# Kernel optimization log

Measured on AMD Instinct MI355X. Metric: run time of the kernel, lower is better.

## Reference

```python
import jax, jax.numpy as jnp
import numpy as np

N_NODES = 1000000
N_EDGES = 2000000
VOCAB = 202        # 200 known codes + 2 specials
MAX_ISN_SIZE = 15
N_REL = 3
DIMS = [36, 24, 16, 8, 4]  # 4 + 32 concat input, then RGCN stack


def setup_inputs() -> dict:
    key = jax.random.key(0)
    ks = jax.random.split(key, 20)
    s = 0.1
    inp = {}
    inp["x_code"] = jax.random.randint(ks[0], (N_NODES,), 0, VOCAB)
    inp["x_size"] = jax.random.randint(ks[1], (N_NODES,), 0, MAX_ISN_SIZE)
    inp["edge_index"] = jax.random.randint(ks[2], (2, N_EDGES), 0, N_NODES)
    inp["edge_type"] = jax.random.randint(ks[3], (N_EDGES,), 0, N_REL)
    inp["size_emb"] = jax.random.normal(ks[4], (MAX_ISN_SIZE, 4), dtype=jnp.float32) * s
    inp["code_emb"] = jax.random.normal(ks[5], (VOCAB, 32), dtype=jnp.float32) * s
    for i in range(4):
        inp[f"w{i}"] = jax.random.normal(ks[6 + 3 * i], (N_REL, DIMS[i], DIMS[i + 1]), dtype=jnp.float32) * s
        inp[f"root{i}"] = jax.random.normal(ks[7 + 3 * i], (DIMS[i], DIMS[i + 1]), dtype=jnp.float32) * s
        inp[f"b{i}"] = jnp.zeros((DIMS[i + 1],), dtype=jnp.float32)
    inp["lin_w"] = jax.random.normal(ks[18], (4, 2), dtype=jnp.float32) * s
    inp["lin_b"] = jnp.zeros((2,), dtype=jnp.float32)
    return inp


def _rgcn(x, src, dst, edge_type, weight, root, bias, n):
    # PyG RGCNConv: out[i] = bias + x[i] @ root + sum_r mean_{j in N_r(i)} x[j] @ W_r
    out = x @ root + bias
    for r in range(N_REL):
        mask = (edge_type == r).astype(x.dtype)            # [E]
        msg = (x @ weight[r])[src] * mask[:, None]          # [E, out]
        ssum = jax.ops.segment_sum(msg, dst, num_segments=n)
        cnt = jax.ops.segment_sum(mask, dst, num_segments=n)
        out = out + ssum / jnp.maximum(cnt, 1.0)[:, None]
    return out


def reference(x_code, x_size, edge_index, edge_type, size_emb, code_emb,
              w0, root0, b0, w1, root1, b1, w2, root2, b2, w3, root3, b3,
              lin_w, lin_b):
    n = x_code.shape[0]
    src, dst = edge_index[0], edge_index[1]
    x = jnp.concatenate([size_emb[x_size], code_emb[x_code]], axis=1)  # [N, 36]
    for w, root, b in ((w0, root0, b0), (w1, root1, b1), (w2, root2, b2), (w3, root3, b3)):
        x = jax.nn.relu(_rgcn(x, src, dst, edge_type, w, root, b, n))
    return x @ lin_w + lin_b  # [N, 2]
```

## Files before the change

### kernel.cpp

```cpp
#include <hip/hip_runtime.h>
#include <hip/hip_fp16.h>

#define NREL 3
#define EPB 2048
#define BKT_SHIFT 10
#define BKT_MASK ((1 << BKT_SHIFT) - 1)

__device__ __forceinline__ void unpack8(uint4 v, float* o) {
    *(float2*)(o+0) = __half22float2(*(__half2*)&v.x);
    *(float2*)(o+2) = __half22float2(*(__half2*)&v.y);
    *(float2*)(o+4) = __half22float2(*(__half2*)&v.z);
    *(float2*)(o+6) = __half22float2(*(__half2*)&v.w);
}
__device__ __forceinline__ unsigned pack2(float a, float b) {
    __half2 h = __floats2half2_rn(a, b);
    return *(unsigned*)&h;
}

__global__ void k_tables2(const float* __restrict__ size_emb,
                          const float* __restrict__ code_emb,
                          const float* __restrict__ w0,
                          const float* __restrict__ root0,
                          const float* __restrict__ b0,
                          float* __restrict__ T, float* __restrict__ Troot,
                          int ns, int nc)
{
    int ntype = ns * nc;
    int tid = blockIdx.x * blockDim.x + threadIdx.x;
    int tot1 = NREL * ntype * 24;
    if (tid < tot1) {
        int d = tid % 24;
        int sc = (tid / 24) % ntype;
        int r = tid / (24 * ntype);
        int sz = sc / nc, cd = sc % nc;
        float a = 0.f;
        #pragma unroll
        for (int k = 0; k < 4; ++k)  a += size_emb[sz*4+k] * w0[(r*36+k)*24+d];
        for (int k = 0; k < 32; ++k) a += code_emb[cd*32+k] * w0[(r*36+4+k)*24+d];
        T[tid] = a;
    } else if (tid < tot1 + ntype * 24) {
        int t = tid - tot1;
        int d = t % 24;
        int sc = t / 24;
        int sz = sc / nc, cd = sc % nc;
        float a = b0[d];
        #pragma unroll
        for (int k = 0; k < 4; ++k)  a += size_emb[sz*4+k] * root0[k*24+d];
        for (int k = 0; k < 32; ++k) a += code_emb[cd*32+k] * root0[(4+k)*24+d];
        Troot[t] = a;
    }
}

__global__ void k_key(const int* __restrict__ x_size, const int* __restrict__ x_code,
                      int* __restrict__ key2, int n, int nc)
{
    int i = blockIdx.x * blockDim.x + threadIdx.x;
    if (i < n) key2[i] = x_size[i] * nc + x_code[i];
}

__global__ void __launch_bounds__(256) k_hist(
    const int* __restrict__ dst, int* __restrict__ histT, int E, int NB, int NBK)
{
    __shared__ int h[1 << BKT_SHIFT];
    int bl = blockIdx.x;
    for (int t = threadIdx.x; t < (1 << BKT_SHIFT); t += 256) h[t] = 0;
    __syncthreads();
    int base = bl * EPB;
    #pragma unroll
    for (int it = 0; it < EPB / 256; ++it) {
        int e = base + it * 256 + (int)threadIdx.x;
        if (e < E) atomicAdd(&h[dst[e] >> BKT_SHIFT], 1);
    }
    __syncthreads();
    for (int b = threadIdx.x; b < NB; b += 256)
        histT[b * NBK + bl] = h[b];
}

__global__ void kscan1(const int* __restrict__ arr, int* __restrict__ partials, int m)
{
    __shared__ int s[256];
    int t = threadIdx.x;
    int base = blockIdx.x * 1024 + t * 4;
    int sum = 0;
    #pragma unroll
    for (int j = 0; j < 4; ++j) {
        int i = base + j;
        if (i < m) sum += arr[i];
    }
    s[t] = sum; __syncthreads();
    for (int off = 128; off > 0; off >>= 1) {
        if (t < off) s[t] += s[t + off];
        __syncthreads();
    }
    if (t == 0) partials[blockIdx.x] = s[0];
}

__global__ void kscan2(int* partials, int np)
{
    __shared__ int s[1024];
    int t = threadIdx.x;
    int v = (t < np) ? partials[t] : 0;
    s[t] = v; __syncthreads();
    for (int off = 1; off < 1024; off <<= 1) {
        int a = (t >= off) ? s[t - off] : 0;
        __syncthreads();
        s[t] += a; __syncthreads();
    }
    if (t < np) partials[t] = s[t] - v;
}

__global__ void kscan3(int* __restrict__ arr, const int* __restrict__ partials, int m)
{
    __shared__ int s[256];
    int t = threadIdx.x;
    int base = blockIdx.x * 1024 + t * 4;
    int d0 = 0, d1 = 0, d2 = 0, d3 = 0;
    if (base + 0 < m) d0 = arr[base+0];
    if (base + 1 < m) d1 = arr[base+1];
    if (base + 2 < m) d2 = arr[base+2];
    if (base + 3 < m) d3 = arr[base+3];
    int tsum = d0 + d1 + d2 + d3;
    s[t] = tsum; __syncthreads();
    for (int off = 1; off < 256; off <<= 1) {
        int a = (t >= off) ? s[t - off] : 0;
        __syncthreads();
        s[t] += a; __syncthreads();
    }
    int excl = s[t] - tsum + partials[blockIdx.x];
    if (base + 0 < m) arr[base+0] = excl;
    if (base + 1 < m) arr[base+1] = excl + d0;
    if (base + 2 < m) arr[base+2] = excl + d0 + d1;
    if (base + 3 < m) arr[base+3] = excl + d0 + d1 + d2;
}

__global__ void __launch_bounds__(256) k_scatter(
    const int* __restrict__ src, const int* __restrict__ dst,
    const int* __restrict__ et, const int* __restrict__ offT,
    unsigned* __restrict__ tmp, int E, int NB, int NBK)
{
    __shared__ int h[1 << BKT_SHIFT];
    int bl = blockIdx.x;
    for (int t = threadIdx.x; t < (1 << BKT_SHIFT); t += 256) h[t] = 0;
    __syncthreads();
    int base = bl * EPB;
    #pragma unroll
    for (int it = 0; it < EPB / 256; ++it) {
        int e = base + it * 256 + (int)threadIdx.x;
        if (e < E) {
            int d = dst[e];
            int b = d >> BKT_SHIFT;
            int rank = atomicAdd(&h[b], 1);
            int pos = offT[b * NBK + bl] + rank;
            tmp[pos] = (unsigned)src[e] | ((unsigned)et[e] << 20)
                     | ((unsigned)(d & BKT_MASK) << 22);
        }
    }
}

__global__ void __launch_bounds__(256) k_csr(
    const unsigned* __restrict__ tmp, const int* __restrict__ offT,
    int* __restrict__ rowptr, unsigned* __restrict__ edges,
    int n, int E, int NB, int NBK)
{
    __shared__ int cnt[1 << BKT_SHIFT];
    __shared__ int fil[1 << BKT_SHIFT];
    __shared__ int ws[256];
    int b = blockIdx.x;
    int eb = offT[b * NBK];
    int ee = (b + 1 < NB) ? offT[(b + 1) * NBK] : E;
    int node0 = b << BKT_SHIFT;

    for (int t = threadIdx.x; t < (1 << BKT_SHIFT); t += 256) cnt[t] = 0;
    __syncthreads();
    for (int e = eb + (int)threadIdx.x; e < ee; e += 256)
        atomicAdd(&cnt[tmp[e] >> 22], 1);
    __syncthreads();

    int t = threadIdx.x;
    int c0 = cnt[4*t+0], c1 = cnt[4*t+1], c2 = cnt[4*t+2], c3 = cnt[4*t+3];
    int tsum = c0 + c1 + c2 + c3;
    ws[t] = tsum; __syncthreads();
    for (int off = 1; off < 256; off <<= 1) {
        int a = (t >= off) ? ws[t - off] : 0;
        __syncthreads();
        ws[t] += a; __syncthreads();
    }
    int excl = ws[t] - tsum;
    fil[4*t+0] = excl;
    fil[4*t+1] = excl + c0;
    fil[4*t+2] = excl + c0 + c1;
    fil[4*t+3] = excl + c0 + c1 + c2;
    __syncthreads();

    for (int l = threadIdx.x; l < (1 << BKT_SHIFT); l += 256) {
        int node = node0 + l;
        if (node < n) rowptr[node] = eb + fil[l];
    }
    if (b == NB - 1 && threadIdx.x == 0) rowptr[n] = E;
    __syncthreads();

    for (int e = eb + (int)threadIdx.x; e < ee; e += 256) {
        unsigned w = tmp[e];
        int l = w >> 22;
        int pos = eb + atomicAdd(&fil[l], 1);
        edges[pos] = w & 0x3FFFFF;
    }
}

__global__ void __launch_bounds__(256) k_layer0_pull(
    const int* __restrict__ key2,
    const int* __restrict__ rowptr, const unsigned* __restrict__ edges,
    const float* __restrict__ T,
    const float* __restrict__ Troot,
    __half* __restrict__ xout, int n, int ntype)
{
    int i = blockIdx.x * blockDim.x + threadIdx.x;
    if (i >= n) return;

    int e0 = rowptr[i], e1 = rowptr[i+1];
    int c0 = 0, c1 = 0, c2 = 0;
    for (int e = e0; e < e1; ++e) {
        int r = edges[e] >> 20;
        c0 += (r == 0); c1 += (r == 1); c2 += (r == 2);
    }
    float inv0 = 1.f / fmaxf((float)c0, 1.f);
    float inv1 = 1.f / fmaxf((float)c1, 1.f);
    float inv2 = 1.f / fmaxf((float)c2, 1.f);

    float acc[24];
    {
        const float4* tr = (const float4*)(Troot + (size_t)key2[i] * 24);
        #pragma unroll
        for (int q = 0; q < 6; ++q) {
            float4 v = tr[q];
            acc[q*4+0]=v.x; acc[q*4+1]=v.y; acc[q*4+2]=v.z; acc[q*4+3]=v.w;
        }
    }
    for (int e = e0; e < e1; ++e) {
        unsigned sl = edges[e];
        int s = sl & 0xFFFFF;
        int r = sl >> 20;
        float w = (r == 0) ? inv0 : ((r == 1) ? inv1 : inv2);
        const float4* trow = (const float4*)(T + ((size_t)r * ntype + key2[s]) * 24);
        #pragma unroll
        for (int q = 0; q < 6; ++q) {
            float4 v = trow[q];
            acc[q*4+0] = fmaf(v.x, w, acc[q*4+0]);
            acc[q*4+1] = fmaf(v.y, w, acc[q*4+1]);
            acc[q*4+2] = fmaf(v.z, w, acc[q*4+2]);
            acc[q*4+3] = fmaf(v.w, w, acc[q*4+3]);
        }
    }
    unsigned ow[12];
    #pragma unroll
    for (int q = 0; q < 12; ++q)
        ow[q] = pack2(fmaxf(acc[2*q], 0.f), fmaxf(acc[2*q+1], 0.f));
    uint4* op = (uint4*)(xout + (size_t)i * 24);
    #pragma unroll
    for (int q = 0; q < 3; ++q) op[q] = ((uint4*)ow)[q];
}

template<int DIN, int DOUT, bool FINAL>
__global__ void __launch_bounds__(256) k_layer_pull(
    const __half* __restrict__ xin,
    __half* __restrict__ xout,
    const int* __restrict__ rowptr, const unsigned* __restrict__ edges,
    const float* __restrict__ W,
    const float* __restrict__ root,
    const float* __restrict__ bias,
    const float* __restrict__ linw,
    const float* __restrict__ linb,
    float* __restrict__ finout, int n)
{
    int j = blockIdx.x * blockDim.x + threadIdx.x;
    if (j >= n) return;

    float a0[DIN], a1[DIN], a2[DIN];
    #pragma unroll
    for (int k = 0; k < DIN; ++k) { a0[k] = 0.f; a1[k] = 0.f; a2[k] = 0.f; }
    int c0 = 0, c1 = 0, c2 = 0;

    int e0 = rowptr[j], e1 = rowptr[j+1];
    for (int e = e0; e < e1; ++e) {
        unsigned sl = edges[e];
        int s = sl & 0xFFFFF;
        int r = sl >> 20;
        const uint4* p = (const uint4*)(xin + (size_t)s * DIN);
        float xs[DIN];
        #pragma unroll
        for (int q = 0; q < DIN/8; ++q) unpack8(p[q], xs + q*8);
        if (r == 0) {
            ++c0;
            #pragma unroll
            for (int k = 0; k < DIN; ++k) a0[k] += xs[k];
        } else if (r == 1) {
            ++c1;
            #pragma unroll
            for (int k = 0; k < DIN; ++k) a1[k] += xs[k];
        } else {
            ++c2;
            #pragma unroll
            for (int k = 0; k < DIN; ++k) a2[k] += xs[k];
        }
    }
    {
        float inv0 = 1.f / fmaxf((float)c0, 1.f);
        float inv1 = 1.f / fmaxf((float)c1, 1.f);
        float inv2 = 1.f / fmaxf((float)c2, 1.f);
        #pragma unroll
        for (int k = 0; k < DIN; ++k) { a0[k] *= inv0; a1[k] *= inv1; a2[k] *= inv2; }
    }

    float o[DOUT];
    #pragma unroll
    for (int d = 0; d < DOUT; ++d) o[d] = bias[d];

    {
        const uint4* p = (const uint4*)(xin + (size_t)j * DIN);
        float xi[DIN];
        #pragma unroll
        for (int q = 0; q < DIN/8; ++q) unpack8(p[q], xi + q*8);
        #pragma unroll
        for (int k = 0; k < DIN; ++k) {
            #pragma unroll
            for (int d = 0; d < DOUT; ++d)
                o[d] = fmaf(xi[k], root[k*DOUT + d], o[d]);
        }
    }
    #pragma unroll
    for (int k = 0; k < DIN; ++k) {
        #pragma unroll
        for (int d = 0; d < DOUT; ++d)
            o[d] = fmaf(a0[k], W[(0*DIN + k)*DOUT + d], o[d]);
    }
    #pragma unroll
    for (int k = 0; k < DIN; ++k) {
        #pragma unroll
        for (int d = 0; d < DOUT; ++d)
            o[d] = fmaf(a1[k], W[(1*DIN + k)*DOUT + d], o[d]);
    }
    #pragma unroll
    for (int k = 0; k < DIN; ++k) {
        #pragma unroll
        for (int d = 0; d < DOUT; ++d)
            o[d] = fmaf(a2[k], W[(2*DIN + k)*DOUT + d], o[d]);
    }
    #pragma unroll
    for (int d = 0; d < DOUT; ++d) o[d] = fmaxf(o[d], 0.f);

    if (FINAL) {
        float o0 = linb[0], o1 = linb[1];
        #pragma unroll
        for (int k = 0; k < 4; ++k) {
            o0 = fmaf(o[k], linw[k*2+0], o0);
            o1 = fmaf(o[k], linw[k*2+1], o1);
        }
        *(float2*)(finout + (size_t)j * 2) = make_float2(o0, o1);
    } else {
        unsigned ow[DOUT/2];
        #pragma unroll
        for (int q = 0; q < DOUT/2; ++q) ow[q] = pack2(o[2*q], o[2*q+1]);
        uint4* op = (uint4*)(xout + (size_t)j * DOUT);
        #pragma unroll
        for (int q = 0; q < DOUT/8; ++q) op[q] = ((uint4*)ow)[q];
    }
}

extern "C" void kernel_launch(void* const* d_in, const int* in_sizes, int n_in,
                              void* d_out, int out_size, void* d_ws, size_t ws_size,
                              hipStream_t stream)
{
    const int*   x_code    = (const int*)d_in[0];
    const int*   x_size    = (const int*)d_in[1];
    const int*   edge_index= (const int*)d_in[2];
    const int*   edge_type = (const int*)d_in[3];
    const float* size_emb  = (const float*)d_in[4];
    const float* code_emb  = (const float*)d_in[5];
    const float* w0 = (const float*)d_in[6];  const float* root0 = (const float*)d_in[7];  const float* b0 = (const float*)d_in[8];
    const float* w1 = (const float*)d_in[9];  const float* root1 = (const float*)d_in[10]; const float* b1 = (const float*)d_in[11];
    const float* w2 = (const float*)d_in[12]; const float* root2 = (const float*)d_in[13]; const float* b2 = (const float*)d_in[14];
    const float* w3 = (const float*)d_in[15]; const float* root3 = (const float*)d_in[16]; const float* b3 = (const float*)d_in[17];
    const float* lin_w = (const float*)d_in[18];
    const float* lin_b = (const float*)d_in[19];

    int n  = in_sizes[0];
    int E  = in_sizes[3];
    int ns = in_sizes[4] / 4;
    int nc = in_sizes[5] / 32;
    int ntype = ns * nc;
    const int* esrc = edge_index;
    const int* edst = edge_index + E;

    int NB  = (n + BKT_MASK) >> BKT_SHIFT;
    int NBK = (E + EPB - 1) / EPB;
    int m   = NB * NBK;

    char* ws = (char*)d_ws;
    size_t off = 0;
    auto alloc = [&](size_t bytes) -> void* {
        void* p = ws + off;
        off = (off + bytes + 255) & ~(size_t)255;
        return p;
    };
    __half*   bufA     = (__half*)  alloc((size_t)n * 24 * 2);
    __half*   bufB     = (__half*)  alloc((size_t)n * 16 * 2);
    int*      rowptr   = (int*)     alloc(((size_t)n + 1) * 4);
    unsigned* edges    = (unsigned*)alloc((size_t)E * 4);
    unsigned* tmp      = (unsigned*)alloc((size_t)E * 4);
    int*      histT    = (int*)     alloc((size_t)m * 4);
    int*      key2     = (int*)     alloc((size_t)n * 4);
    int*      partials = (int*)     alloc(4096 * 4);
    float*    T        = (float*)   alloc((size_t)NREL * ntype * 24 * 4);
    float*    Troot    = (float*)   alloc((size_t)ntype * 24 * 4);

    const int tb = 256;
    int tableThreads = NREL*ntype*24 + ntype*24;
    k_tables2<<<(tableThreads + tb - 1)/tb, tb, 0, stream>>>(
        size_emb, code_emb, w0, root0, b0, T, Troot, ns, nc);
    k_key<<<(n + tb - 1)/tb, tb, 0, stream>>>(x_size, x_code, key2, n, nc);

    k_hist<<<NBK, tb, 0, stream>>>(edst, histT, E, NB, NBK);
    int nblk = (m + 1023) / 1024;
    kscan1<<<nblk, tb, 0, stream>>>(histT, partials, m);
    kscan2<<<1, 1024, 0, stream>>>(partials, nblk);
    kscan3<<<nblk, tb, 0, stream>>>(histT, partials, m);
    k_scatter<<<NBK, tb, 0, stream>>>(esrc, edst, edge_type, histT, tmp, E, NB, NBK);
    k_csr<<<NB, tb, 0, stream>>>(tmp, histT, rowptr, edges, n, E, NB, NBK);

    int g256 = (n + 255) / 256;
    k_layer0_pull<<<g256, tb, 0, stream>>>(key2, rowptr, edges, T, Troot, bufA, n, ntype);
    k_layer_pull<24,16,false><<<g256, tb, 0, stream>>>(bufA, bufB, rowptr, edges,
                                                 w1, root1, b1, nullptr, nullptr, nullptr, n);
    k_layer_pull<16, 8,false><<<g256, tb, 0, stream>>>(bufB, bufA, rowptr, edges,
                                                 w2, root2, b2, nullptr, nullptr, nullptr, n);
    k_layer_pull< 8, 4,true ><<<g256, tb, 0, stream>>>(bufA, nullptr, rowptr, edges,
                                                 w3, root3, b3, lin_w, lin_b, (float*)d_out, n);
}
```

Before: 432.6 us.

## Precompute source type keys into compact edge array and widen buckets

The scatter pass now looks up each edge's source type key once and packs it, together with the relation, into a 16-bit per-edge array that layer 0 reads. This removes layer 0's dependent random gather of key2[src]. Buckets widen from 1024 to 4096 nodes, so the histogram uses 256 bins and the CSR build scans 16 counts per thread. Layer-1 input rows are padded to 32 halves (64 B) for aligned gathers, which adds memory traffic, and the scatter pass does extra random reads and writes 8-byte temp entries.

```diff
diff --git a/kernel.cpp b/kernel.cpp
--- a/kernel.cpp
+++ b/kernel.cpp
@@ -3,8 +3,10 @@
 
 #define NREL 3
 #define EPB 2048
-#define BKT_SHIFT 10
-#define BKT_MASK ((1 << BKT_SHIFT) - 1)
+#define BKT_SHIFT 12
+#define BKT_NODES (1 << BKT_SHIFT)
+#define BKT_MASK (BKT_NODES - 1)
+#define X1S 32
 
 __device__ __forceinline__ void unpack8(uint4 v, float* o) {
     *(float2*)(o+0) = __half22float2(*(__half2*)&v.x);
@@ -61,9 +63,9 @@
 __global__ void __launch_bounds__(256) k_hist(
     const int* __restrict__ dst, int* __restrict__ histT, int E, int NB, int NBK)
 {
-    __shared__ int h[1 << BKT_SHIFT];
+    __shared__ int h[256];
     int bl = blockIdx.x;
-    for (int t = threadIdx.x; t < (1 << BKT_SHIFT); t += 256) h[t] = 0;
+    h[threadIdx.x] = 0;
     __syncthreads();
     int base = bl * EPB;
     #pragma unroll
@@ -72,8 +74,8 @@
         if (e < E) atomicAdd(&h[dst[e] >> BKT_SHIFT], 1);
     }
     __syncthreads();
-    for (int b = threadIdx.x; b < NB; b += 256)
-        histT[b * NBK + bl] = h[b];
+    if ((int)threadIdx.x < NB)
+        histT[threadIdx.x * NBK + bl] = h[threadIdx.x];
 }
 
 __global__ void kscan1(const int* __restrict__ arr, int* __restrict__ partials, int m)
@@ -135,12 +137,13 @@
 
 __global__ void __launch_bounds__(256) k_scatter(
     const int* __restrict__ src, const int* __restrict__ dst,
-    const int* __restrict__ et, const int* __restrict__ offT,
-    unsigned* __restrict__ tmp, int E, int NB, int NBK)
-{
-    __shared__ int h[1 << BKT_SHIFT];
+    const int* __restrict__ et, const int* __restrict__ key2,
+    const int* __restrict__ offT,
+    uint2* __restrict__ tmp, int E, int NB, int NBK)
+{
+    __shared__ int h[256];
     int bl = blockIdx.x;
-    for (int t = threadIdx.x; t < (1 << BKT_SHIFT); t += 256) h[t] = 0;
+    h[threadIdx.x] = 0;
     __syncthreads();
     int base = bl * EPB;
     #pragma unroll
@@ -149,67 +152,80 @@
         if (e < E) {
             int d = dst[e];
             int b = d >> BKT_SHIFT;
+            int s = src[e];
+            int r = et[e];
+            int tk = key2[s];
             int rank = atomicAdd(&h[b], 1);
             int pos = offT[b * NBK + bl] + rank;
-            tmp[pos] = (unsigned)src[e] | ((unsigned)et[e] << 20)
-                     | ((unsigned)(d & BKT_MASK) << 22);
+            tmp[pos] = make_uint2((unsigned)s | ((unsigned)r << 20),
+                                  (unsigned)(d & BKT_MASK)
+                                | ((unsigned)tk << 12)
+                                | ((unsigned)r << 24));
         }
     }
 }
 
 __global__ void __launch_bounds__(256) k_csr(
-    const unsigned* __restrict__ tmp, const int* __restrict__ offT,
+    const uint2* __restrict__ tmp, const int* __restrict__ offT,
     int* __restrict__ rowptr, unsigned* __restrict__ edges,
+    unsigned short* __restrict__ edges0,
     int n, int E, int NB, int NBK)
 {
-    __shared__ int cnt[1 << BKT_SHIFT];
-    __shared__ int fil[1 << BKT_SHIFT];
+    __shared__ int cnt[BKT_NODES];
+    __shared__ int fil[BKT_NODES];
     __shared__ int ws[256];
     int b = blockIdx.x;
     int eb = offT[b * NBK];
     int ee = (b + 1 < NB) ? offT[(b + 1) * NBK] : E;
     int node0 = b << BKT_SHIFT;
-
-    for (int t = threadIdx.x; t < (1 << BKT_SHIFT); t += 256) cnt[t] = 0;
-    __syncthreads();
-    for (int e = eb + (int)threadIdx.x; e < ee; e += 256)
-        atomicAdd(&cnt[tmp[e] >> 22], 1);
-    __syncthreads();
-
     int t = threadIdx.x;
-    int c0 = cnt[4*t+0], c1 = cnt[4*t+1], c2 = cnt[4*t+2], c3 = cnt[4*t+3];
-    int tsum = c0 + c1 + c2 + c3;
-    ws[t] = tsum; __syncthreads();
-    for (int off = 1; off < 256; off <<= 1) {
-        int a = (t >= off) ? ws[t - off] : 0;
-        __syncthreads();
-        ws[t] += a; __syncthreads();
-    }
-    int excl = ws[t] - tsum;
-    fil[4*t+0] = excl;
-    fil[4*t+1] = excl + c0;
-    fil[4*t+2] = excl + c0 + c1;
-    fil[4*t+3] = excl + c0 + c1 + c2;
-    __syncthreads();
-
-    for (int l = threadIdx.x; l < (1 << BKT_SHIFT); l += 256) {
+
+    for (int l = t; l < BKT_NODES; l += 256) cnt[l] = 0;
+    __syncthreads();
+    for (int e = eb + t; e < ee; e += 256)
+        atomicAdd(&cnt[tmp[e].y & BKT_MASK], 1);
+    __syncthreads();
+
+    {
+        int base16 = t * 16;
+        int sum = 0;
+        #pragma unroll
+        for (int j = 0; j < 16; ++j) sum += cnt[base16 + j];
+        ws[t] = sum; __syncthreads();
+        for (int off = 1; off < 256; off <<= 1) {
+            int a = (t >= off) ? ws[t - off] : 0;
+            __syncthreads();
+            ws[t] += a; __syncthreads();
+        }
+        int run = ws[t] - sum;
+        #pragma unroll
+        for (int j = 0; j < 16; ++j) {
+            int c = cnt[base16 + j];
+            fil[base16 + j] = run;
+            run += c;
+        }
+    }
+    __syncthreads();
+
+    for (int l = t; l < BKT_NODES; l += 256) {
         int node = node0 + l;
         if (node < n) rowptr[node] = eb + fil[l];
     }
-    if (b == NB - 1 && threadIdx.x == 0) rowptr[n] = E;
-    __syncthreads();
-
-    for (int e = eb + (int)threadIdx.x; e < ee; e += 256) {
-        unsigned w = tmp[e];
-        int l = w >> 22;
+    if (b == NB - 1 && t == 0) rowptr[n] = E;
+    __syncthreads();
+
+    for (int e = eb + t; e < ee; e += 256) {
+        uint2 w = tmp[e];
+        int l = w.y & BKT_MASK;
         int pos = eb + atomicAdd(&fil[l], 1);
-        edges[pos] = w & 0x3FFFFF;
+        edges[pos]  = w.x;
+        edges0[pos] = (unsigned short)(w.y >> 12);
     }
 }
 
 __global__ void __launch_bounds__(256) k_layer0_pull(
     const int* __restrict__ key2,
-    const int* __restrict__ rowptr, const unsigned* __restrict__ edges,
+    const int* __restrict__ rowptr, const unsigned short* __restrict__ edges0,
     const float* __restrict__ T,
     const float* __restrict__ Troot,
     __half* __restrict__ xout, int n, int ntype)
@@ -220,7 +236,7 @@
     int e0 = rowptr[i], e1 = rowptr[i+1];
     int c0 = 0, c1 = 0, c2 = 0;
     for (int e = e0; e < e1; ++e) {
-        int r = edges[e] >> 20;
+        int r = edges0[e] >> 12;
         c0 += (r == 0); c1 += (r == 1); c2 += (r == 2);
     }
     float inv0 = 1.f / fmaxf((float)c0, 1.f);
@@ -237,11 +253,11 @@
         }
     }
     for (int e = e0; e < e1; ++e) {
-        unsigned sl = edges[e];
-        int s = sl & 0xFFFFF;
-        int r = sl >> 20;
+        unsigned short sl = edges0[e];
+        int tk = sl & 0xFFF;
+        int r  = sl >> 12;
         float w = (r == 0) ? inv0 : ((r == 1) ? inv1 : inv2);
-        const float4* trow = (const float4*)(T + ((size_t)r * ntype + key2[s]) * 24);
+        const float4* trow = (const float4*)(T + ((size_t)r * ntype + tk) * 24);
         #pragma unroll
         for (int q = 0; q < 6; ++q) {
             float4 v = trow[q];
@@ -251,16 +267,17 @@
             acc[q*4+3] = fmaf(v.w, w, acc[q*4+3]);
         }
     }
-    unsigned ow[12];
+    unsigned ow[16];
     #pragma unroll
     for (int q = 0; q < 12; ++q)
         ow[q] = pack2(fmaxf(acc[2*q], 0.f), fmaxf(acc[2*q+1], 0.f));
-    uint4* op = (uint4*)(xout + (size_t)i * 24);
-    #pragma unroll
-    for (int q = 0; q < 3; ++q) op[q] = ((uint4*)ow)[q];
-}
-
-template<int DIN, int DOUT, bool FINAL>
+    ow[12] = ow[13] = ow[14] = ow[15] = 0;
+    uint4* op = (uint4*)(xout + (size_t)i * X1S);
+    #pragma unroll
+    for (int q = 0; q < 4; ++q) op[q] = ((uint4*)ow)[q];
+}
+
+template<int DIN, int DINS, int DOUT, bool FINAL>
 __global__ void __launch_bounds__(256) k_layer_pull(
     const __half* __restrict__ xin,
     __half* __restrict__ xout,
@@ -285,7 +302,7 @@
         unsigned sl = edges[e];
         int s = sl & 0xFFFFF;
         int r = sl >> 20;
-        const uint4* p = (const uint4*)(xin + (size_t)s * DIN);
+        const uint4* p = (const uint4*)(xin + (size_t)s * DINS);
         float xs[DIN];
         #pragma unroll
         for (int q = 0; q < DIN/8; ++q) unpack8(p[q], xs + q*8);
@@ -316,7 +333,7 @@
     for (int d = 0; d < DOUT; ++d) o[d] = bias[d];
 
     {
-        const uint4* p = (const uint4*)(xin + (size_t)j * DIN);
+        const uint4* p = (const uint4*)(xin + (size_t)j * DINS);
         float xi[DIN];
         #pragma unroll
         for (int q = 0; q < DIN/8; ++q) unpack8(p[q], xi + q*8);
@@ -402,16 +419,17 @@
         off = (off + bytes + 255) & ~(size_t)255;
         return p;
     };
-    __half*   bufA     = (__half*)  alloc((size_t)n * 24 * 2);
-    __half*   bufB     = (__half*)  alloc((size_t)n * 16 * 2);
-    int*      rowptr   = (int*)     alloc(((size_t)n + 1) * 4);
-    unsigned* edges    = (unsigned*)alloc((size_t)E * 4);
-    unsigned* tmp      = (unsigned*)alloc((size_t)E * 4);
-    int*      histT    = (int*)     alloc((size_t)m * 4);
-    int*      key2     = (int*)     alloc((size_t)n * 4);
-    int*      partials = (int*)     alloc(4096 * 4);
-    float*    T        = (float*)   alloc((size_t)NREL * ntype * 24 * 4);
-    float*    Troot    = (float*)   alloc((size_t)ntype * 24 * 4);
+    __half*         bufA   = (__half*)        alloc((size_t)n * X1S * 2);
+    __half*         bufB   = (__half*)        alloc((size_t)n * 16 * 2);
+    int*            rowptr = (int*)           alloc(((size_t)n + 1) * 4);
+    unsigned*       edges  = (unsigned*)      alloc((size_t)E * 4);
+    unsigned short* edges0 = (unsigned short*)alloc((size_t)E * 2);
+    uint2*          tmp    = (uint2*)         alloc((size_t)E * 8);
+    int*            histT  = (int*)           alloc((size_t)m * 4);
+    int*            key2   = (int*)           alloc((size_t)n * 4);
+    int*            partials=(int*)           alloc(4096 * 4);
+    float*          T      = (float*)         alloc((size_t)NREL * ntype * 24 * 4);
+    float*          Troot  = (float*)         alloc((size_t)ntype * 24 * 4);
 
     const int tb = 256;
     int tableThreads = NREL*ntype*24 + ntype*24;
@@ -424,15 +442,15 @@
     kscan1<<<nblk, tb, 0, stream>>>(histT, partials, m);
     kscan2<<<1, 1024, 0, stream>>>(partials, nblk);
     kscan3<<<nblk, tb, 0, stream>>>(histT, partials, m);
-    k_scatter<<<NBK, tb, 0, stream>>>(esrc, edst, edge_type, histT, tmp, E, NB, NBK);
-    k_csr<<<NB, tb, 0, stream>>>(tmp, histT, rowptr, edges, n, E, NB, NBK);
+    k_scatter<<<NBK, tb, 0, stream>>>(esrc, edst, edge_type, key2, histT, tmp, E, NB, NBK);
+    k_csr<<<NB, tb, 0, stream>>>(tmp, histT, rowptr, edges, edges0, n, E, NB, NBK);
 
     int g256 = (n + 255) / 256;
-    k_layer0_pull<<<g256, tb, 0, stream>>>(key2, rowptr, edges, T, Troot, bufA, n, ntype);
-    k_layer_pull<24,16,false><<<g256, tb, 0, stream>>>(bufA, bufB, rowptr, edges,
+    k_layer0_pull<<<g256, tb, 0, stream>>>(key2, rowptr, edges0, T, Troot, bufA, n, ntype);
+    k_layer_pull<24,X1S,16,false><<<g256, tb, 0, stream>>>(bufA, bufB, rowptr, edges,
                                                  w1, root1, b1, nullptr, nullptr, nullptr, n);
-    k_layer_pull<16, 8,false><<<g256, tb, 0, stream>>>(bufB, bufA, rowptr, edges,
+    k_layer_pull<16,16, 8,false><<<g256, tb, 0, stream>>>(bufB, bufA, rowptr, edges,
                                                  w2, root2, b2, nullptr, nullptr, nullptr, n);
-    k_layer_pull< 8, 4,true ><<<g256, tb, 0, stream>>>(bufA, nullptr, rowptr, edges,
+    k_layer_pull< 8, 8, 4,true ><<<g256, tb, 0, stream>>>(bufA, nullptr, rowptr, edges,
                                                  w3, root3, b3, lin_w, lin_b, (float*)d_out, n);
 }
```

New measurement: 436.4 us. No clear change (+0.9%).
